# Optimization experiments

Hardware: AMD Instinct MI355X
Metric: run time of the kernel (lower is better)

Reference implementation:

```python
import jax, jax.numpy as jnp
import numpy as np

N_NODES = 100000
N_EDGES = 1600000
NODE_DIM = 32
MSG_DIM = 32
COORD_DIM = 3
FF_HALF = 4  # FourierLayer(1, 8) -> coeff [1, 4]


def silu(x):
    return x * jax.nn.sigmoid(x)


def setup_inputs() -> dict:
    key = jax.random.key(0)
    ks = jax.random.split(key, 16)
    s = lambda fan_in: 1.0 / np.sqrt(fan_in)
    edge_in = 2 * NODE_DIM + 2 * FF_HALF  # 72
    node_in = MSG_DIM + NODE_DIM          # 64
    return {
        "coord": jax.random.normal(ks[0], (N_NODES, COORD_DIM), jnp.float32),
        "node_feat": jax.random.normal(ks[1], (N_NODES, NODE_DIM), jnp.float32),
        "edge_index": jax.random.randint(ks[2], (2, N_EDGES), 0, N_NODES, jnp.int64 if jax.config.jax_enable_x64 else jnp.int32),
        "ff_coeff": jax.random.normal(ks[3], (1, FF_HALF), jnp.float32),  # sigma=1.0
        "ew1": jax.random.uniform(ks[4], (edge_in, MSG_DIM), jnp.float32, -s(edge_in), s(edge_in)),
        "eb1": jax.random.uniform(ks[5], (MSG_DIM,), jnp.float32, -s(edge_in), s(edge_in)),
        "ew2": jax.random.uniform(ks[6], (MSG_DIM, MSG_DIM), jnp.float32, -s(MSG_DIM), s(MSG_DIM)),
        "eb2": jax.random.uniform(ks[7], (MSG_DIM,), jnp.float32, -s(MSG_DIM), s(MSG_DIM)),
        "cw1": jax.random.uniform(ks[8], (MSG_DIM, MSG_DIM), jnp.float32, -s(MSG_DIM), s(MSG_DIM)),
        "cb1": jax.random.uniform(ks[9], (MSG_DIM,), jnp.float32, -s(MSG_DIM), s(MSG_DIM)),
        "cw2": jax.random.uniform(ks[10], (MSG_DIM, 1), jnp.float32, -s(MSG_DIM), s(MSG_DIM)),  # bias-free last coord layer
        "nw1": jax.random.uniform(ks[11], (node_in, MSG_DIM), jnp.float32, -s(node_in), s(node_in)),
        "nb1": jax.random.uniform(ks[12], (MSG_DIM,), jnp.float32, -s(node_in), s(node_in)),
        "nw2": jax.random.uniform(ks[13], (MSG_DIM, NODE_DIM), jnp.float32, -s(MSG_DIM), s(MSG_DIM)),
        "nb2": jax.random.uniform(ks[14], (NODE_DIM,), jnp.float32, -s(MSG_DIM), s(MSG_DIM)),
    }


def reference(coord, node_feat, edge_index, ff_coeff, ew1, eb1, ew2, eb2,
              cw1, cb1, cw2, nw1, nb1, nw2, nb2):
    n = coord.shape[0]
    idx_i, idx_j = edge_index[0], edge_index[1]
    # coord2radial (sparse, normalize=False)
    coord_diff = coord[idx_i] - coord[idx_j]                 # [E, 3]
    radial = jnp.sum(coord_diff * coord_diff, axis=1, keepdims=True)  # [E, 1]
    # Fourier radial features (ffr=True): ff1(radial) -> [E, 8]
    x_proj = (2.0 * jnp.pi) * (radial @ ff_coeff)            # [E, 4]
    ff = jnp.concatenate([jnp.cos(x_proj), jnp.sin(x_proj)], axis=-1)  # [E, 8]
    # edge MLP
    edge_in = jnp.concatenate([node_feat[idx_i], node_feat[idx_j], ff], axis=1)  # [E, 72]
    m = silu(edge_in @ ew1 + eb1)
    m = silu(m @ ew2 + eb2)                                  # [E, M]
    # coord model: per-edge scalar weight on coord_diff, mean-aggregated to nodes
    w = silu(m @ cw1 + cb1) @ cw2                            # [E, 1]
    trans = coord_diff * w                                   # [E, 3]
    agg_c = jax.ops.segment_sum(trans, idx_i, num_segments=n)
    counts = jax.ops.segment_sum(jnp.ones((trans.shape[0],), trans.dtype), idx_i, num_segments=n)
    coord_out = coord + agg_c / jnp.clip(counts, 1.0)[:, None]
    # node model: sum-aggregated messages, residual
    agg_h = jax.ops.segment_sum(m, idx_i, num_segments=n)    # [N, M]
    h = silu(jnp.concatenate([node_feat, agg_h], axis=1) @ nw1 + nb1)
    h = h @ nw2 + nb2
    node_out = node_feat + h                                 # is_residual=True
    return node_out, coord_out
```

## Files before the change

### kernel.cpp

```cpp
#include <hip/hip_runtime.h>
#include <math.h>

#ifndef M_PIf
#define M_PIf 3.14159265358979323846f
#endif

__device__ __forceinline__ float silu_f(float x) {
    return x / (1.0f + __expf(-x));
}

__device__ __forceinline__ void edge_core(
    const float* __restrict__ coord,
    const float* __restrict__ node_feat,
    const float* __restrict__ ff_coeff,
    const float* __restrict__ ew1, const float* __restrict__ eb1,
    const float* __restrict__ ew2, const float* __restrict__ eb2,
    const float* __restrict__ cw1, const float* __restrict__ cb1,
    const float* __restrict__ cw2,
    int i, int j,
    float* __restrict__ m,
    float& cdx, float& cdy, float& cdz, float& w)
{
    const float cix = coord[3*(size_t)i+0], ciy = coord[3*(size_t)i+1], ciz = coord[3*(size_t)i+2];
    const float cjx = coord[3*(size_t)j+0], cjy = coord[3*(size_t)j+1], cjz = coord[3*(size_t)j+2];
    cdx = cix - cjx; cdy = ciy - cjy; cdz = ciz - cjz;
    const float radial = cdx*cdx + cdy*cdy + cdz*cdz;

    float ff[8];
    #pragma unroll
    for (int k = 0; k < 4; ++k) {
        float xp = (2.0f * M_PIf) * radial * ff_coeff[k];
        float s, c;
        sincosf(xp, &s, &c);
        ff[k]     = c;
        ff[4 + k] = s;
    }

    float acc[32];
    #pragma unroll
    for (int o = 0; o < 32; ++o) acc[o] = eb1[o];

    {
        const float4* nfi4 = reinterpret_cast<const float4*>(node_feat + (size_t)i * 32);
        for (int q = 0; q < 8; ++q) {
            float4 v = nfi4[q];
            float xs[4] = {v.x, v.y, v.z, v.w};
            const float* wr = ew1 + q * 4 * 32;
            #pragma unroll
            for (int kk = 0; kk < 4; ++kk) {
                #pragma unroll
                for (int o = 0; o < 32; ++o)
                    acc[o] = fmaf(xs[kk], wr[kk*32 + o], acc[o]);
            }
        }
        const float4* nfj4 = reinterpret_cast<const float4*>(node_feat + (size_t)j * 32);
        for (int q = 0; q < 8; ++q) {
            float4 v = nfj4[q];
            float xs[4] = {v.x, v.y, v.z, v.w};
            const float* wr = ew1 + (32 + q * 4) * 32;
            #pragma unroll
            for (int kk = 0; kk < 4; ++kk) {
                #pragma unroll
                for (int o = 0; o < 32; ++o)
                    acc[o] = fmaf(xs[kk], wr[kk*32 + o], acc[o]);
            }
        }
        #pragma unroll
        for (int k = 0; k < 8; ++k) {
            const float* wr = ew1 + (64 + k) * 32;
            #pragma unroll
            for (int o = 0; o < 32; ++o)
                acc[o] = fmaf(ff[k], wr[o], acc[o]);
        }
    }

    float m1[32];
    #pragma unroll
    for (int o = 0; o < 32; ++o) m1[o] = silu_f(acc[o]);

    #pragma unroll
    for (int o = 0; o < 32; ++o) m[o] = eb2[o];
    #pragma unroll
    for (int h = 0; h < 32; ++h) {
        #pragma unroll
        for (int o = 0; o < 32; ++o)
            m[o] = fmaf(m1[h], ew2[h*32 + o], m[o]);
    }
    #pragma unroll
    for (int o = 0; o < 32; ++o) m[o] = silu_f(m[o]);

    float c1[32];
    #pragma unroll
    for (int o = 0; o < 32; ++o) c1[o] = cb1[o];
    #pragma unroll
    for (int h = 0; h < 32; ++h) {
        #pragma unroll
        for (int o = 0; o < 32; ++o)
            c1[o] = fmaf(m[h], cw1[h*32 + o], c1[o]);
    }
    w = 0.0f;
    #pragma unroll
    for (int o = 0; o < 32; ++o) w += silu_f(c1[o]) * cw2[o];
}


__global__ __launch_bounds__(256) void egc_hist(
    const int* __restrict__ idx_i, int* __restrict__ counts, int E)
{
    const int e = blockIdx.x * 256 + threadIdx.x;
    if (e < E) atomicAdd(&counts[idx_i[e]], 1);
}

__global__ __launch_bounds__(1024) void egc_scan(
    const int* __restrict__ counts, int* __restrict__ row_start,
    int* __restrict__ cursor, int N)
{
    __shared__ int wsum[16];
    __shared__ int carry_s;
    const int tid = threadIdx.x;
    const int lane = tid & 63, wid = tid >> 6;
    if (tid == 0) carry_s = 0;
    __syncthreads();
    for (int base = 0; base < N; base += 1024) {
        const int idx = base + tid;
        const int x = (idx < N) ? counts[idx] : 0;
        int incl = x;
        #pragma unroll
        for (int off = 1; off < 64; off <<= 1) {
            int v = __shfl_up(incl, off, 64);
            if (lane >= off) incl += v;
        }
        if (lane == 63) wsum[wid] = incl;
        __syncthreads();
        if (wid == 0) {
            int v = (lane < 16) ? wsum[lane] : 0;
            int s = v;
            #pragma unroll
            for (int off = 1; off < 16; off <<= 1) {
                int t = __shfl_up(s, off, 64);
                if (lane >= off) s += t;
            }
            if (lane < 16) wsum[lane] = s - v;
        }
        __syncthreads();
        const int carry = carry_s;
        if (idx < N) {
            const int v = carry + wsum[wid] + incl - x;
            row_start[idx] = v;
            cursor[idx]    = v;
        }
        __syncthreads();
        if (tid == 1023) carry_s = carry + wsum[15] + incl;
        __syncthreads();
    }
    if (tid == 0) row_start[N] = carry_s;
}

__global__ __launch_bounds__(256) void egc_edge_direct(
    const float* __restrict__ coord,
    const float* __restrict__ node_feat,
    const int*   __restrict__ edge_index,
    const float* __restrict__ ff_coeff,
    const float* __restrict__ ew1, const float* __restrict__ eb1,
    const float* __restrict__ ew2, const float* __restrict__ eb2,
    const float* __restrict__ cw1, const float* __restrict__ cb1,
    const float* __restrict__ cw2,
    int*   __restrict__ cursor,
    float* __restrict__ m_buf,
    float* __restrict__ trans4,
    int E)
{
    const int e = blockIdx.x * 256 + threadIdx.x;
    if (e >= E) return;

    const int i = edge_index[e];
    const int j = edge_index[E + e];
    const int slot = atomicAdd(&cursor[i], 1);

    float m[32], cdx, cdy, cdz, w;
    edge_core(coord, node_feat, ff_coeff, ew1, eb1, ew2, eb2, cw1, cb1, cw2,
              i, j, m, cdx, cdy, cdz, w);

    float4* mb = reinterpret_cast<float4*>(m_buf + (size_t)slot * 32);
    #pragma unroll
    for (int q = 0; q < 8; ++q) {
        float4 v;
        v.x = m[4*q+0]; v.y = m[4*q+1]; v.z = m[4*q+2]; v.w = m[4*q+3];
        mb[q] = v;
    }
    float4 t; t.x = cdx * w; t.y = cdy * w; t.z = cdz * w; t.w = 0.0f;
    *reinterpret_cast<float4*>(trans4 + (size_t)slot * 4) = t;
}

__global__ __launch_bounds__(256) void egc_node_direct(
    const float* __restrict__ coord,
    const float* __restrict__ node_feat,
    const float* __restrict__ m_buf,
    const float* __restrict__ trans4,
    const int*   __restrict__ row_start,
    const float* __restrict__ nw1, const float* __restrict__ nb1,
    const float* __restrict__ nw2, const float* __restrict__ nb2,
    float* __restrict__ out_node,
    float* __restrict__ out_coord,
    int N)
{
    const int n = blockIdx.x * 256 + threadIdx.x;
    if (n >= N) return;

    const int rs = row_start[n];
    const int re = row_start[n + 1];

    float agg[32];
    #pragma unroll
    for (int o = 0; o < 32; ++o) agg[o] = 0.0f;
    float acx = 0.0f, acy = 0.0f, acz = 0.0f;

    for (int k = rs; k < re; ++k) {
        const float4* mb = reinterpret_cast<const float4*>(m_buf + (size_t)k * 32);
        #pragma unroll
        for (int q = 0; q < 8; ++q) {
            float4 v = mb[q];
            agg[4*q+0] += v.x; agg[4*q+1] += v.y; agg[4*q+2] += v.z; agg[4*q+3] += v.w;
        }
        float4 t = *reinterpret_cast<const float4*>(trans4 + (size_t)k * 4);
        acx += t.x; acy += t.y; acz += t.z;
    }

    float nf[32];
    {
        const float4* nf4 = reinterpret_cast<const float4*>(node_feat + (size_t)n * 32);
        #pragma unroll
        for (int q = 0; q < 8; ++q) {
            float4 v = nf4[q];
            nf[4*q+0] = v.x; nf[4*q+1] = v.y; nf[4*q+2] = v.z; nf[4*q+3] = v.w;
        }
    }

    float acc[32];
    #pragma unroll
    for (int o = 0; o < 32; ++o) acc[o] = nb1[o];
    #pragma unroll
    for (int k = 0; k < 32; ++k) {
        #pragma unroll
        for (int o = 0; o < 32; ++o)
            acc[o] = fmaf(nf[k], nw1[k*32 + o], acc[o]);
    }
    #pragma unroll
    for (int k = 0; k < 32; ++k) {
        #pragma unroll
        for (int o = 0; o < 32; ++o)
            acc[o] = fmaf(agg[k], nw1[(32+k)*32 + o], acc[o]);
    }
    float h1[32];
    #pragma unroll
    for (int o = 0; o < 32; ++o) h1[o] = silu_f(acc[o]);

    float h2[32];
    #pragma unroll
    for (int o = 0; o < 32; ++o) h2[o] = nb2[o];
    #pragma unroll
    for (int k = 0; k < 32; ++k) {
        #pragma unroll
        for (int o = 0; o < 32; ++o)
            h2[o] = fmaf(h1[k], nw2[k*32 + o], h2[o]);
    }

    {
        float4* on4 = reinterpret_cast<float4*>(out_node + (size_t)n * 32);
        #pragma unroll
        for (int q = 0; q < 8; ++q) {
            float4 v;
            v.x = nf[4*q+0] + h2[4*q+0];
            v.y = nf[4*q+1] + h2[4*q+1];
            v.z = nf[4*q+2] + h2[4*q+2];
            v.w = nf[4*q+3] + h2[4*q+3];
            on4[q] = v;
        }
    }

    const float deg = (float)(re - rs);
    const float inv = 1.0f / fmaxf(deg, 1.0f);
    out_coord[(size_t)n*3 + 0] = coord[(size_t)n*3 + 0] + acx * inv;
    out_coord[(size_t)n*3 + 1] = coord[(size_t)n*3 + 1] + acy * inv;
    out_coord[(size_t)n*3 + 2] = coord[(size_t)n*3 + 2] + acz * inv;
}


__global__ __launch_bounds__(256) void egc_edge_fb(
    const float* __restrict__ coord,
    const float* __restrict__ node_feat,
    const int*   __restrict__ edge_index,
    const float* __restrict__ ff_coeff,
    const float* __restrict__ ew1, const float* __restrict__ eb1,
    const float* __restrict__ ew2, const float* __restrict__ eb2,
    const float* __restrict__ cw1, const float* __restrict__ cb1,
    const float* __restrict__ cw2,
    float* __restrict__ agg_h, float* __restrict__ agg_c, float* __restrict__ counts,
    int E)
{
    const int e = blockIdx.x * 256 + threadIdx.x;
    if (e >= E) return;
    const int i = edge_index[e];
    const int j = edge_index[E + e];

    float m[32], cdx, cdy, cdz, w;
    edge_core(coord, node_feat, ff_coeff, ew1, eb1, ew2, eb2, cw1, cb1, cw2,
              i, j, m, cdx, cdy, cdz, w);

    float* dst = agg_h + (size_t)i * 32;
    #pragma unroll
    for (int o = 0; o < 32; ++o) atomicAdd(&dst[o], m[o]);
    atomicAdd(&agg_c[(size_t)i*3 + 0], cdx * w);
    atomicAdd(&agg_c[(size_t)i*3 + 1], cdy * w);
    atomicAdd(&agg_c[(size_t)i*3 + 2], cdz * w);
    atomicAdd(&counts[i], 1.0f);
}

__global__ __launch_bounds__(256) void egc_node_fb(
    const float* __restrict__ coord,
    const float* __restrict__ node_feat,
    const float* __restrict__ agg_h,
    const float* __restrict__ agg_c,
    const float* __restrict__ counts,
    const float* __restrict__ nw1, const float* __restrict__ nb1,
    const float* __restrict__ nw2, const float* __restrict__ nb2,
    float* __restrict__ out_node, float* __restrict__ out_coord, int N)
{
    const int n = blockIdx.x * 256 + threadIdx.x;
    if (n >= N) return;

    float nf[32];
    {
        const float4* nf4 = reinterpret_cast<const float4*>(node_feat + (size_t)n * 32);
        #pragma unroll
        for (int q = 0; q < 8; ++q) {
            float4 v = nf4[q];
            nf[4*q+0] = v.x; nf[4*q+1] = v.y; nf[4*q+2] = v.z; nf[4*q+3] = v.w;
        }
    }
    float acc[32];
    #pragma unroll
    for (int o = 0; o < 32; ++o) acc[o] = nb1[o];
    #pragma unroll
    for (int k = 0; k < 32; ++k) {
        #pragma unroll
        for (int o = 0; o < 32; ++o)
            acc[o] = fmaf(nf[k], nw1[k*32 + o], acc[o]);
    }
    {
        const float4* ah4 = reinterpret_cast<const float4*>(agg_h + (size_t)n * 32);
        #pragma unroll
        for (int q = 0; q < 8; ++q) {
            float4 v = ah4[q];
            float xs[4] = {v.x, v.y, v.z, v.w};
            const float* wr = nw1 + (32 + q * 4) * 32;
            #pragma unroll
            for (int kk = 0; kk < 4; ++kk) {
                #pragma unroll
                for (int o = 0; o < 32; ++o)
                    acc[o] = fmaf(xs[kk], wr[kk*32 + o], acc[o]);
            }
        }
    }
    float h1[32];
    #pragma unroll
    for (int o = 0; o < 32; ++o) h1[o] = silu_f(acc[o]);
    float h2[32];
    #pragma unroll
    for (int o = 0; o < 32; ++o) h2[o] = nb2[o];
    #pragma unroll
    for (int k = 0; k < 32; ++k) {
        #pragma unroll
        for (int o = 0; o < 32; ++o)
            h2[o] = fmaf(h1[k], nw2[k*32 + o], h2[o]);
    }
    {
        float4* on4 = reinterpret_cast<float4*>(out_node + (size_t)n * 32);
        #pragma unroll
        for (int q = 0; q < 8; ++q) {
            float4 v;
            v.x = nf[4*q+0] + h2[4*q+0];
            v.y = nf[4*q+1] + h2[4*q+1];
            v.z = nf[4*q+2] + h2[4*q+2];
            v.w = nf[4*q+3] + h2[4*q+3];
            on4[q] = v;
        }
    }
    const float cnt = fmaxf(counts[n], 1.0f);
    const float inv = 1.0f / cnt;
    out_coord[(size_t)n*3 + 0] = coord[(size_t)n*3 + 0] + agg_c[(size_t)n*3 + 0] * inv;
    out_coord[(size_t)n*3 + 1] = coord[(size_t)n*3 + 1] + agg_c[(size_t)n*3 + 1] * inv;
    out_coord[(size_t)n*3 + 2] = coord[(size_t)n*3 + 2] + agg_c[(size_t)n*3 + 2] * inv;
}


extern "C" void kernel_launch(void* const* d_in, const int* in_sizes, int n_in,
                              void* d_out, int out_size, void* d_ws, size_t ws_size,
                              hipStream_t stream) {
    const float* coord     = (const float*)d_in[0];
    const float* node_feat = (const float*)d_in[1];
    const int*   edge_index= (const int*)  d_in[2];
    const float* ff_coeff  = (const float*)d_in[3];
    const float* ew1 = (const float*)d_in[4];
    const float* eb1 = (const float*)d_in[5];
    const float* ew2 = (const float*)d_in[6];
    const float* eb2 = (const float*)d_in[7];
    const float* cw1 = (const float*)d_in[8];
    const float* cb1 = (const float*)d_in[9];
    const float* cw2 = (const float*)d_in[10];
    const float* nw1 = (const float*)d_in[11];
    const float* nb1 = (const float*)d_in[12];
    const float* nw2 = (const float*)d_in[13];
    const float* nb2 = (const float*)d_in[14];

    const int N = in_sizes[0] / 3;
    const int E = in_sizes[2] / 2;

    float* out_node  = (float*)d_out;
    float* out_coord = out_node + (size_t)N * 32;

    const size_t m_off   = 0;
    const size_t t_off   = m_off + (size_t)E * 32;
    const size_t cnt_off = t_off + (size_t)E * 4;
    const size_t cur_off = cnt_off + (size_t)N;
    const size_t rs_off  = cur_off + (size_t)N;
    const size_t need_bytes = (rs_off + (size_t)N + 1) * 4 + 256;

    if (ws_size >= need_bytes) {
        float* m_buf     = (float*)d_ws + m_off;
        float* trans4    = (float*)d_ws + t_off;
        int*   counts    = (int*)d_ws + cnt_off;
        int*   cursor    = (int*)d_ws + cur_off;
        int*   row_start = (int*)d_ws + rs_off;

        hipMemsetAsync(counts, 0, (size_t)N * sizeof(int), stream);

        egc_hist<<<(E + 255) / 256, 256, 0, stream>>>(edge_index, counts, E);

        egc_scan<<<1, 1024, 0, stream>>>(counts, row_start, cursor, N);

        egc_edge_direct<<<(E + 255) / 256, 256, 0, stream>>>(
            coord, node_feat, edge_index, ff_coeff,
            ew1, eb1, ew2, eb2, cw1, cb1, cw2,
            cursor, m_buf, trans4, E);

        egc_node_direct<<<(N + 255) / 256, 256, 0, stream>>>(
            coord, node_feat, m_buf, trans4, row_start,
            nw1, nb1, nw2, nb2, out_node, out_coord, N);
    } else {
        float* agg_h  = (float*)d_ws;
        float* agg_c  = agg_h + (size_t)N * 32;
        float* counts = agg_c + (size_t)N * 3;
        hipMemsetAsync(d_ws, 0, (size_t)N * 36 * sizeof(float), stream);

        egc_edge_fb<<<(E + 255) / 256, 256, 0, stream>>>(
            coord, node_feat, edge_index, ff_coeff,
            ew1, eb1, ew2, eb2, cw1, cb1, cw2,
            agg_h, agg_c, counts, E);

        egc_node_fb<<<(N + 255) / 256, 256, 0, stream>>>(
            coord, node_feat, agg_h, agg_c, counts,
            nw1, nb1, nw2, nb2, out_node, out_coord, N);
    }
}
```

Before: 818.9 us.

## Map each node to 32 lanes, use hardware sincos, scatter trans by edge id

The node kernel now gives each node 32 lanes instead of one thread. Each lane sums one message channel over the node's CSR range and computes one output column of the node MLP, using lane shuffles to broadcast inputs. The edge kernel writes trans4 coalesced by edge index and records a slot-to-edge permutation that the node kernel follows with an indirect load. The Fourier features use the AMD hardware sin/cos builtins on a revolution-normalized argument instead of full-precision sincosf, which lowers accuracy for large arguments.

```diff
diff --git a/kernel.cpp b/kernel.cpp
--- a/kernel.cpp
+++ b/kernel.cpp
@@ -1,12 +1,19 @@
 #include <hip/hip_runtime.h>
 #include <math.h>
 
-#ifndef M_PIf
-#define M_PIf 3.14159265358979323846f
-#endif
-
 __device__ __forceinline__ float silu_f(float x) {
     return x / (1.0f + __expf(-x));
+}
+
+__device__ __forceinline__ void sincos_2pi_rev(float rev, float& s, float& c) {
+#if __has_builtin(__builtin_amdgcn_sinf) && __has_builtin(__builtin_amdgcn_cosf)
+    const float fr = rev - floorf(rev);
+    s = __builtin_amdgcn_sinf(fr);
+    c = __builtin_amdgcn_cosf(fr);
+#else
+    const float xp = 6.2831853071795864769f * rev;
+    s = sinf(xp); c = cosf(xp);
+#endif
 }
 
 __device__ __forceinline__ void edge_core(
@@ -29,9 +36,8 @@
     float ff[8];
     #pragma unroll
     for (int k = 0; k < 4; ++k) {
-        float xp = (2.0f * M_PIf) * radial * ff_coeff[k];
         float s, c;
-        sincosf(xp, &s, &c);
+        sincos_2pi_rev(radial * ff_coeff[k], s, c);
         ff[k]     = c;
         ff[4 + k] = s;
     }
@@ -168,6 +174,7 @@
     int*   __restrict__ cursor,
     float* __restrict__ m_buf,
     float* __restrict__ trans4,
+    int*   __restrict__ eord,
     int E)
 {
     const int e = blockIdx.x * 256 + threadIdx.x;
@@ -189,14 +196,16 @@
         mb[q] = v;
     }
     float4 t; t.x = cdx * w; t.y = cdy * w; t.z = cdz * w; t.w = 0.0f;
-    *reinterpret_cast<float4*>(trans4 + (size_t)slot * 4) = t;
-}
-
-__global__ __launch_bounds__(256) void egc_node_direct(
+    *reinterpret_cast<float4*>(trans4 + (size_t)e * 4) = t;
+    eord[slot] = e;
+}
+
+__global__ __launch_bounds__(256) void egc_node_wave(
     const float* __restrict__ coord,
     const float* __restrict__ node_feat,
     const float* __restrict__ m_buf,
     const float* __restrict__ trans4,
+    const int*   __restrict__ eord,
     const int*   __restrict__ row_start,
     const float* __restrict__ nw1, const float* __restrict__ nb1,
     const float* __restrict__ nw2, const float* __restrict__ nb2,
@@ -204,85 +213,47 @@
     float* __restrict__ out_coord,
     int N)
 {
-    const int n = blockIdx.x * 256 + threadIdx.x;
+    const int tid = threadIdx.x;
+    const int l32 = tid & 31;
+    const int n = blockIdx.x * 8 + (tid >> 5);
     if (n >= N) return;
 
     const int rs = row_start[n];
     const int re = row_start[n + 1];
 
-    float agg[32];
-    #pragma unroll
-    for (int o = 0; o < 32; ++o) agg[o] = 0.0f;
-    float acx = 0.0f, acy = 0.0f, acz = 0.0f;
-
+    float agg = 0.0f;
+    float tr  = 0.0f;
     for (int k = rs; k < re; ++k) {
-        const float4* mb = reinterpret_cast<const float4*>(m_buf + (size_t)k * 32);
-        #pragma unroll
-        for (int q = 0; q < 8; ++q) {
-            float4 v = mb[q];
-            agg[4*q+0] += v.x; agg[4*q+1] += v.y; agg[4*q+2] += v.z; agg[4*q+3] += v.w;
-        }
-        float4 t = *reinterpret_cast<const float4*>(trans4 + (size_t)k * 4);
-        acx += t.x; acy += t.y; acz += t.z;
-    }
-
-    float nf[32];
-    {
-        const float4* nf4 = reinterpret_cast<const float4*>(node_feat + (size_t)n * 32);
-        #pragma unroll
-        for (int q = 0; q < 8; ++q) {
-            float4 v = nf4[q];
-            nf[4*q+0] = v.x; nf[4*q+1] = v.y; nf[4*q+2] = v.z; nf[4*q+3] = v.w;
-        }
-    }
-
-    float acc[32];
-    #pragma unroll
-    for (int o = 0; o < 32; ++o) acc[o] = nb1[o];
-    #pragma unroll
-    for (int k = 0; k < 32; ++k) {
-        #pragma unroll
-        for (int o = 0; o < 32; ++o)
-            acc[o] = fmaf(nf[k], nw1[k*32 + o], acc[o]);
-    }
-    #pragma unroll
-    for (int k = 0; k < 32; ++k) {
-        #pragma unroll
-        for (int o = 0; o < 32; ++o)
-            acc[o] = fmaf(agg[k], nw1[(32+k)*32 + o], acc[o]);
-    }
-    float h1[32];
-    #pragma unroll
-    for (int o = 0; o < 32; ++o) h1[o] = silu_f(acc[o]);
-
-    float h2[32];
-    #pragma unroll
-    for (int o = 0; o < 32; ++o) h2[o] = nb2[o];
-    #pragma unroll
-    for (int k = 0; k < 32; ++k) {
-        #pragma unroll
-        for (int o = 0; o < 32; ++o)
-            h2[o] = fmaf(h1[k], nw2[k*32 + o], h2[o]);
-    }
-
-    {
-        float4* on4 = reinterpret_cast<float4*>(out_node + (size_t)n * 32);
-        #pragma unroll
-        for (int q = 0; q < 8; ++q) {
-            float4 v;
-            v.x = nf[4*q+0] + h2[4*q+0];
-            v.y = nf[4*q+1] + h2[4*q+1];
-            v.z = nf[4*q+2] + h2[4*q+2];
-            v.w = nf[4*q+3] + h2[4*q+3];
-            on4[q] = v;
-        }
-    }
-
-    const float deg = (float)(re - rs);
-    const float inv = 1.0f / fmaxf(deg, 1.0f);
-    out_coord[(size_t)n*3 + 0] = coord[(size_t)n*3 + 0] + acx * inv;
-    out_coord[(size_t)n*3 + 1] = coord[(size_t)n*3 + 1] + acy * inv;
-    out_coord[(size_t)n*3 + 2] = coord[(size_t)n*3 + 2] + acz * inv;
+        agg += m_buf[(size_t)k * 32 + l32];
+        if (l32 < 3) {
+            const int e = eord[k];
+            tr += trans4[(size_t)e * 4 + l32];
+        }
+    }
+
+    const float nf = node_feat[(size_t)n * 32 + l32];
+
+    float acc = nb1[l32];
+    #pragma unroll
+    for (int k = 0; k < 32; ++k)
+        acc = fmaf(__shfl(nf, k, 32), nw1[k*32 + l32], acc);
+    #pragma unroll
+    for (int k = 0; k < 32; ++k)
+        acc = fmaf(__shfl(agg, k, 32), nw1[(32+k)*32 + l32], acc);
+    const float h1 = silu_f(acc);
+
+    float h2 = nb2[l32];
+    #pragma unroll
+    for (int k = 0; k < 32; ++k)
+        h2 = fmaf(__shfl(h1, k, 32), nw2[k*32 + l32], h2);
+
+    out_node[(size_t)n * 32 + l32] = nf + h2;
+
+    if (l32 < 3) {
+        const float deg = (float)(re - rs);
+        out_coord[(size_t)n * 3 + l32] =
+            coord[(size_t)n * 3 + l32] + tr / fmaxf(deg, 1.0f);
+    }
 }
 
 
@@ -421,7 +392,8 @@
 
     const size_t m_off   = 0;
     const size_t t_off   = m_off + (size_t)E * 32;
-    const size_t cnt_off = t_off + (size_t)E * 4;
+    const size_t eo_off  = t_off + (size_t)E * 4;
+    const size_t cnt_off = eo_off + (size_t)E;
     const size_t cur_off = cnt_off + (size_t)N;
     const size_t rs_off  = cur_off + (size_t)N;
     const size_t need_bytes = (rs_off + (size_t)N + 1) * 4 + 256;
@@ -429,6 +401,7 @@
     if (ws_size >= need_bytes) {
         float* m_buf     = (float*)d_ws + m_off;
         float* trans4    = (float*)d_ws + t_off;
+        int*   eord      = (int*)d_ws + eo_off;
         int*   counts    = (int*)d_ws + cnt_off;
         int*   cursor    = (int*)d_ws + cur_off;
         int*   row_start = (int*)d_ws + rs_off;
@@ -442,10 +415,10 @@
         egc_edge_direct<<<(E + 255) / 256, 256, 0, stream>>>(
             coord, node_feat, edge_index, ff_coeff,
             ew1, eb1, ew2, eb2, cw1, cb1, cw2,
-            cursor, m_buf, trans4, E);
-
-        egc_node_direct<<<(N + 255) / 256, 256, 0, stream>>>(
-            coord, node_feat, m_buf, trans4, row_start,
+            cursor, m_buf, trans4, eord, E);
+
+        egc_node_wave<<<(N + 7) / 8, 256, 0, stream>>>(
+            coord, node_feat, m_buf, trans4, eord, row_start,
             nw1, nb1, nw2, nb2, out_node, out_coord, N);
     } else {
         float* agg_h  = (float*)d_ws;
```

After: 861.3 us. +5.2%, slower.
